# Optimization experiments

Measured on AMD Instinct MI355X. Metric: run time of the kernel, lower is better.

Reference implementation:

```python
import math
import jax, jax.numpy as jnp
import numpy as np

HEADS = 8
LOG_APPROX_VAR = math.log(0.01)  # self.var = 0.01, non-trainable


def clustering(x, approx_log_var, mu, log_var, log_prior):
    """Faithful port of DisentangledAttention.clustering (mi_estimation=False).
    x: [B,H,L,D]; approx_log_var: [B,H,L]; mu/log_var: [H,C,D]; log_prior: [H,C].
    Returns (cluster_probs [B,H,L,C], kl_loss [B,1,1], div_loss [B])."""
    B, H, L, D = x.shape
    xe = x[:, :, :, None, :]                      # [B,H,L,1,D]
    mue = mu[:, None, :, :]                       # [H,1,C,D]
    alv = approx_log_var[:, :, :, None, None]     # [B,H,L,1,1]
    avar = jnp.exp(alv)
    lv = log_var[:, None, :, :]                   # [H,1,C,D]
    var = jnp.exp(lv)
    logp = jax.nn.log_softmax(log_prior, axis=-1)  # [H,C]

    mse = (xe - mue) ** 2 / var                   # [B,H,L,C,D]
    log_pdf = -0.5 * mse.sum(-1) - D * math.pi - 0.5 * lv.sum(-1)  # [B,H,L,C]
    log_pdf = log_pdf + logp[:, None, :]
    log_probs = jax.nn.log_softmax(log_pdf, axis=-1)
    probs = jnp.exp(log_probs)                    # [B,H,L,C]

    logp_b = logp[None, :, None, :]               # broadcast prior log-probs
    prior = jnp.exp(logp_b)
    # F.kl_div(log_probs, prior) = prior * (log(prior) - log_probs)
    kl = (prior * (logp_b - log_probs)).sum(-1).mean(axis=(1, 2))            # [B]
    kl = kl + 0.5 * (probs * (mse + avar / var + lv).sum(-1)).sum(-1).mean(axis=(1, 2))
    kl = kl - 0.5 * jnp.mean(((1.0 + alv).sum(-1)) * D, axis=(1, 2, 3))
    kl_loss = kl.reshape(-1, 1, 1)

    eyeL = jnp.eye(L, dtype=x.dtype)
    div = jnp.einsum('bhqc,bhkc->bhqk', probs, probs)   # [B,H,L,L]
    div = (div - eyeL) ** 2
    wmask = eyeL * 1.25 + (1.0 - eyeL) * 0.75
    div_loss = (div * wmask).mean(axis=(1, 2, 3))       # [B]
    return probs, kl_loss, div_loss


def setup_inputs() -> dict:
    k = jax.random.key(0)
    ks = jax.random.split(k, 10)
    B, L, D, H, C = 4, 1024, 512, HEADS, 8
    Dk = D // H
    lin_std = 1.0 / math.sqrt(2.0 * D)  # xavier_normal gain=1/sqrt(2)
    return {
        'query': jax.random.normal(ks[0], (B, L, D), jnp.float32),
        'key': jax.random.normal(ks[1], (B, L, D), jnp.float32),
        'value': jax.random.normal(ks[2], (B, L, D), jnp.float32),
        'padding_mask': jnp.zeros((B, 1, L), jnp.float32),
        'Wq': jax.random.normal(ks[3], (D, D), jnp.float32) * lin_std,
        'bq': jnp.zeros((D,), jnp.float32),
        'Wk': jax.random.normal(ks[4], (D, D), jnp.float32) * lin_std,
        'bk': jnp.zeros((D,), jnp.float32),
        'Wv': jax.random.normal(ks[5], (D, D), jnp.float32) * lin_std,
        'bv': jnp.zeros((D,), jnp.float32),
        'Wo': jax.random.normal(ks[6], (D, D), jnp.float32) * lin_std,
        'bo': jnp.zeros((D,), jnp.float32),
        'tok_mu': jax.random.normal(ks[7], (H, C, Dk), jnp.float32) * 0.1,
        'tok_log_var': jnp.zeros((H, C, Dk), jnp.float32),
        'tok_log_prior': jnp.full((H, C), math.log(1.0 / C), jnp.float32),
    }


def reference(query, key, value, padding_mask, Wq, bq, Wk, bk, Wv, bv, Wo, bo,
              tok_mu, tok_log_var, tok_log_prior):
    B, L, D = query.shape
    H = HEADS
    Dk = D // H

    # GMM clustering on raw (unprojected) per-head query/key, eval mode (no reparam noise)
    qh = query.reshape(B, L, H, Dk).transpose(0, 2, 1, 3)  # [B,H,L,Dk]
    kh = key.reshape(B, L, H, Dk).transpose(0, 2, 1, 3)
    alv = jnp.full((B, H, L), LOG_APPROX_VAR, dtype=query.dtype)
    probs_q, kl_q, div_q = clustering(qh, alv, tok_mu, tok_log_var, tok_log_prior)
    probs_k, kl_k, div_k = clustering(kh, alv, tok_mu, tok_log_var, tok_log_prior)

    # Disentangled mask: tokens sharing clusters attend (mask==1 means blocked)
    sim = jnp.einsum('bhqc,bhkc->bhqk', probs_q, probs_k)   # [B,H,L,L]
    cmask = jnp.clip(1.0 - sim + padding_mask[:, :, None, :], 0.0, 1.0)

    # Projections + scaled softmax attention (per softmax_attention/full_attention)
    q = (query @ Wq.T + bq).reshape(B, L, H, Dk).transpose(0, 2, 1, 3) / math.sqrt(Dk)
    kk = (key @ Wk.T + bk).reshape(B, L, H, Dk).transpose(0, 2, 1, 3)
    v = (value @ Wv.T + bv).reshape(B, L, H, Dk).transpose(0, 2, 1, 3)
    scores = jnp.einsum('bhqd,bhkd->bhqk', q, kk) + jax.lax.stop_gradient(cmask) * (-10000.0)
    attn = jax.nn.softmax(scores, axis=-1) * (1.0 - cmask)
    out = jnp.einsum('bhqk,bhkd->bhqd', attn, v).transpose(0, 2, 1, 3).reshape(B, L, D)
    out = out @ Wo.T + bo

    kl_loss = kl_q + kl_k                      # [B,1,1]
    div_loss = (div_q + div_k).reshape(-1, 1, 1)  # [B,1,1]
    return out, kl_loss, div_loss
```

## Files before the change

kernel.cpp:

```cpp
#include <hip/hip_runtime.h>
#include <hip/hip_bf16.h>
#include <math.h>

#define NB 4
#define NL 1024
#define ND 512
#define NH 8
#define NC 8
#define NDK 64

static constexpr float KL3_CONST = 115.36544595161891f;

typedef __bf16 bf16x8 __attribute__((ext_vector_type(8)));
typedef float  f32x4v __attribute__((ext_vector_type(4)));
typedef unsigned short u16x4 __attribute__((ext_vector_type(4)));
typedef unsigned short u16x8 __attribute__((ext_vector_type(8)));

__device__ __forceinline__ unsigned short bf16u(float f) {
    return __builtin_bit_cast(unsigned short, (__bf16)f);
}

struct GemmArgs {
    const void* A; const float* W; const float* bias; void* out;
    float scale; int abf; int obf; int brow; int ostr; int vmap;
};

#define GEMM_BUF 15360

__device__ __forceinline__ void gemm_body(const GemmArgs& g, unsigned char* smem)
{
    const int tid = threadIdx.x;
    int n0, m0;
    if (g.vmap) {
        const int linear = blockIdx.y * 4 + blockIdx.x;
        n0 = (linear & 31) * 128;
        m0 = (linear >> 5) * 64;
    } else {
        n0 = blockIdx.x * 128;
        m0 = blockIdx.y * 64;
    }

    const int w = tid >> 6, lane = tid & 63;
    const int r16 = lane & 15, quad = lane >> 4;
    const int arow = tid >> 2, akc = tid & 3;
    const int wrow = tid >> 1, wkc = tid & 1;

    f32x4v acc[8];
#pragma unroll
    for (int n = 0; n < 8; ++n) acc[n] = (f32x4v){0.f, 0.f, 0.f, 0.f};

    auto ldA = [&](int k0) -> u16x8 {
        if (g.abf) {
            return *(const u16x8*)((const unsigned short*)g.A + (size_t)(m0 + arow) * 512 + k0 + akc * 8);
        }
        const float* ap = (const float*)g.A + (size_t)(m0 + arow) * 512 + k0 + akc * 8;
        const float4 a0 = *(const float4*)ap, a1 = *(const float4*)(ap + 4);
        return (u16x8){ bf16u(a0.x), bf16u(a0.y), bf16u(a0.z), bf16u(a0.w),
                        bf16u(a1.x), bf16u(a1.y), bf16u(a1.z), bf16u(a1.w) };
    };
    auto ldW = [&](int k0, u16x8* dst) {
        const float* wp = (const float*)g.W + (size_t)(n0 + wrow) * 512 + k0 + wkc * 16;
        const float4 w0 = *(const float4*)wp,       w1 = *(const float4*)(wp + 4);
        const float4 w2 = *(const float4*)(wp + 8), w3 = *(const float4*)(wp + 12);
        dst[0] = (u16x8){ bf16u(w0.x), bf16u(w0.y), bf16u(w0.z), bf16u(w0.w),
                          bf16u(w1.x), bf16u(w1.y), bf16u(w1.z), bf16u(w1.w) };
        dst[1] = (u16x8){ bf16u(w2.x), bf16u(w2.y), bf16u(w2.z), bf16u(w2.w),
                          bf16u(w3.x), bf16u(w3.y), bf16u(w3.z), bf16u(w3.w) };
    };
    auto store_stage = [&](int buf, const u16x8& sa, const u16x8* sw) {
        unsigned short* As = (unsigned short*)(smem + buf * GEMM_BUF);
        unsigned short* Ws = (unsigned short*)(smem + buf * GEMM_BUF + 5120);
        *(u16x8*)(As + arow * 40 + akc * 8) = sa;
        *(u16x8*)(Ws + wrow * 40 + wkc * 16) = sw[0];
        *(u16x8*)(Ws + wrow * 40 + wkc * 16 + 8) = sw[1];
    };
    auto mfma_half = [&](int buf) {
        unsigned short* As = (unsigned short*)(smem + buf * GEMM_BUF);
        unsigned short* Ws = (unsigned short*)(smem + buf * GEMM_BUF + 5120);
        bf16x8 af = *(const bf16x8*)(As + (w * 16 + r16) * 40 + quad * 8);
#pragma unroll
        for (int ni = 0; ni < 8; ++ni) {
            bf16x8 bfr = *(const bf16x8*)(Ws + (ni * 16 + r16) * 40 + quad * 8);
            acc[ni] = __builtin_amdgcn_mfma_f32_16x16x32_bf16(af, bfr, acc[ni], 0, 0, 0);
        }
    };

    u16x8 sa0 = ldA(0),  sw0[2]; ldW(0, sw0);
    u16x8 sa1 = ldA(32), sw1[2]; ldW(32, sw1);
    store_stage(0, sa0, sw0);
    sa0 = ldA(64); ldW(64, sw0);

    for (int p = 0; p < 16; p += 2) {
        const int kbase = p * 32;
        __syncthreads();
        store_stage(1, sa1, sw1);
        if (kbase + 96 < 512) { sa1 = ldA(kbase + 96); ldW(kbase + 96, sw1); }
        mfma_half(0);

        __syncthreads();
        if (p + 2 < 16) store_stage(0, sa0, sw0);
        if (kbase + 128 < 512) { sa0 = ldA(kbase + 128); ldW(kbase + 128, sw0); }
        mfma_half(1);
    }

#pragma unroll
    for (int ni = 0; ni < 8; ++ni) {
        const int col = n0 + ni * 16 + r16;
        const float bcol = g.brow ? 0.f : g.bias[col];
#pragma unroll
        for (int i = 0; i < 4; ++i) {
            const int row = m0 + w * 16 + quad * 4 + i;
            const float bv = g.brow ? g.bias[row] : bcol;
            const float v = (acc[ni][i] + bv) * g.scale;
            if (g.obf) ((unsigned short*)g.out)[(size_t)row * g.ostr + col] = bf16u(v);
            else       ((float*)g.out)[(size_t)row * g.ostr + col] = v;
        }
    }
}

#define GEMM_BUF64 10240

__device__ __forceinline__ void gemm_body64(const GemmArgs& g, unsigned char* smem)
{
    const int tid = threadIdx.x;
    const int n0 = blockIdx.x * 64, m0 = blockIdx.y * 64;

    const int w = tid >> 6, lane = tid & 63;
    const int r16 = lane & 15, quad = lane >> 4;
    const int arow = tid >> 2, akc = tid & 3;

    f32x4v acc[4];
#pragma unroll
    for (int n = 0; n < 4; ++n) acc[n] = (f32x4v){0.f, 0.f, 0.f, 0.f};

    auto ldA = [&](int k0) -> u16x8 {
        if (g.abf) {
            return *(const u16x8*)((const unsigned short*)g.A + (size_t)(m0 + arow) * 512 + k0 + akc * 8);
        }
        const float* ap = (const float*)g.A + (size_t)(m0 + arow) * 512 + k0 + akc * 8;
        const float4 a0 = *(const float4*)ap, a1 = *(const float4*)(ap + 4);
        return (u16x8){ bf16u(a0.x), bf16u(a0.y), bf16u(a0.z), bf16u(a0.w),
                        bf16u(a1.x), bf16u(a1.y), bf16u(a1.z), bf16u(a1.w) };
    };
    auto ldW8 = [&](int k0) -> u16x8 {
        const float* wp = (const float*)g.W + (size_t)(n0 + arow) * 512 + k0 + akc * 8;
        const float4 w0 = *(const float4*)wp, w1 = *(const float4*)(wp + 4);
        return (u16x8){ bf16u(w0.x), bf16u(w0.y), bf16u(w0.z), bf16u(w0.w),
                        bf16u(w1.x), bf16u(w1.y), bf16u(w1.z), bf16u(w1.w) };
    };
    auto store_stage = [&](int buf, const u16x8& sa, const u16x8& sw) {
        unsigned short* As = (unsigned short*)(smem + buf * GEMM_BUF64);
        unsigned short* Ws = (unsigned short*)(smem + buf * GEMM_BUF64 + 5120);
        *(u16x8*)(As + arow * 40 + akc * 8) = sa;
        *(u16x8*)(Ws + arow * 40 + akc * 8) = sw;
    };
    auto mfma_half = [&](int buf) {
        unsigned short* As = (unsigned short*)(smem + buf * GEMM_BUF64);
        unsigned short* Ws = (unsigned short*)(smem + buf * GEMM_BUF64 + 5120);
        bf16x8 af = *(const bf16x8*)(As + (w * 16 + r16) * 40 + quad * 8);
#pragma unroll
        for (int ni = 0; ni < 4; ++ni) {
            bf16x8 bfr = *(const bf16x8*)(Ws + (ni * 16 + r16) * 40 + quad * 8);
            acc[ni] = __builtin_amdgcn_mfma_f32_16x16x32_bf16(af, bfr, acc[ni], 0, 0, 0);
        }
    };

    u16x8 sa0 = ldA(0),  sw0 = ldW8(0);
    u16x8 sa1 = ldA(32), sw1 = ldW8(32);
    store_stage(0, sa0, sw0);
    sa0 = ldA(64); sw0 = ldW8(64);

    for (int p = 0; p < 16; p += 2) {
        const int kbase = p * 32;
        __syncthreads();
        store_stage(1, sa1, sw1);
        if (kbase + 96 < 512) { sa1 = ldA(kbase + 96); sw1 = ldW8(kbase + 96); }
        mfma_half(0);

        __syncthreads();
        if (p + 2 < 16) store_stage(0, sa0, sw0);
        if (kbase + 128 < 512) { sa0 = ldA(kbase + 128); sw0 = ldW8(kbase + 128); }
        mfma_half(1);
    }

#pragma unroll
    for (int ni = 0; ni < 4; ++ni) {
        const int col = n0 + ni * 16 + r16;
        const float bcol = g.brow ? 0.f : g.bias[col];
#pragma unroll
        for (int i = 0; i < 4; ++i) {
            const int row = m0 + w * 16 + quad * 4 + i;
            const float bv = g.brow ? g.bias[row] : bcol;
            const float v = (acc[ni][i] + bv) * g.scale;
            if (g.obf) ((unsigned short*)g.out)[(size_t)row * g.ostr + col] = bf16u(v);
            else       ((float*)g.out)[(size_t)row * g.ostr + col] = v;
        }
    }
}

__device__ __forceinline__ void cluster_body(
    const float* __restrict__ query, const float* __restrict__ key,
    const float* __restrict__ tok_mu, const float* __restrict__ tok_log_var,
    const float* __restrict__ tok_log_prior,
    float* __restrict__ probs_q, float* __restrict__ probs_k,
    float* __restrict__ klp, float* __restrict__ divp, float* __restrict__ Gp,
    int linear, unsigned char* smem)
{
    float* mu_s    = (float*)smem;
    float* iv_s    = (float*)(smem + 2048);
    float* Pl      = (float*)(smem + 4096);
    float* Gpart   = (float*)(smem + 13312);
    float* red_s   = (float*)(smem + 14336);
    float* lvsum_s = (float*)(smem + 14368);
    float* alpha_s = (float*)(smem + 14400);
    float* logp_s  = (float*)(smem + 14432);
    float* prior_s = (float*)(smem + 14464);

    const int tid  = threadIdx.x;
    const int side = linear >> 7;
    const int rem  = linear & 127;
    const int bh   = rem >> 2, chunk = rem & 3;
    const int b    = bh >> 3, h = bh & 7;
    const int blocklin = side * 128 + bh * 4 + chunk;
    const float* src = side ? key : query;
    float* probs_out = side ? probs_k : probs_q;

    for (int i = tid; i < 512; i += 256) {
        mu_s[i] = tok_mu[h * 512 + i];
        float lv = tok_log_var[h * 512 + i];
        iv_s[i] = __expf(-lv);
    }
    if (tid < 8) {
        float ls = 0.f, al = 0.f;
        for (int d = 0; d < 64; ++d) {
            float lv = tok_log_var[(h * 8 + tid) * 64 + d];
            ls += lv;
            al += 0.01f * __expf(-lv) + lv;
        }
        lvsum_s[tid] = ls; alpha_s[tid] = al;
    }
    if (tid == 0) {
        float lp[8]; float mx = -1e30f;
        for (int c = 0; c < 8; ++c) { lp[c] = tok_log_prior[h * 8 + c]; mx = fmaxf(mx, lp[c]); }
        float se = 0.f;
        for (int c = 0; c < 8; ++c) se += __expf(lp[c] - mx);
        float lse = mx + __logf(se);
        for (int c = 0; c < 8; ++c) { logp_s[c] = lp[c] - lse; prior_s[c] = __expf(lp[c] - lse); }
    }
    __syncthreads();

    const int l = chunk * 256 + tid;
    const float4* xp = (const float4*)(src + ((size_t)(b * NL + l)) * ND + h * NDK);
    float4 xr[16];
#pragma unroll
    for (int i = 0; i < 16; ++i) xr[i] = xp[i];

    float ms[8];
#pragma unroll
    for (int c = 0; c < 8; ++c) {
        const float4* mc = (const float4*)(mu_s + c * 64);
        const float4* ic = (const float4*)(iv_s + c * 64);
        float s = 0.f;
#pragma unroll
        for (int i = 0; i < 16; ++i) {
            float4 m4 = mc[i], v4 = ic[i], x4 = xr[i];
            float dx = x4.x - m4.x; s = fmaf(dx * dx, v4.x, s);
            float dy = x4.y - m4.y; s = fmaf(dy * dy, v4.y, s);
            float dz = x4.z - m4.z; s = fmaf(dz * dz, v4.z, s);
            float dw = x4.w - m4.w; s = fmaf(dw * dw, v4.w, s);
        }
        ms[c] = s;
    }

    float lpdf[8]; float mx = -1e30f;
#pragma unroll
    for (int c = 0; c < 8; ++c) {
        lpdf[c] = -0.5f * (ms[c] + lvsum_s[c]) + logp_s[c];
        mx = fmaxf(mx, lpdf[c]);
    }
    float e[8]; float se = 0.f;
#pragma unroll
    for (int c = 0; c < 8; ++c) { e[c] = __expf(lpdf[c] - mx); se += e[c]; }
    float lse = __logf(se);
    float inv = 1.f / se;
    float p[8]; float kl1 = 0.f, kl2 = 0.f, sqq = 0.f;
#pragma unroll
    for (int c = 0; c < 8; ++c) {
        p[c] = e[c] * inv;
        float logprob = lpdf[c] - mx - lse;
        kl1 += prior_s[c] * (logp_s[c] - logprob);
        kl2 += p[c] * (ms[c] + alpha_s[c]);
        sqq = fmaf(p[c], p[c], sqq);
    }

    float* po = probs_out + ((size_t)((b * NH + h) * NL + l)) * NC;
    ((float4*)po)[0] = make_float4(p[0], p[1], p[2], p[3]);
    ((float4*)po)[1] = make_float4(p[4], p[5], p[6], p[7]);
#pragma unroll
    for (int c = 0; c < 8; ++c) Pl[tid * 9 + c] = p[c];

    float dterm = 1.25f * (sqq - 1.f) * (sqq - 1.f) - 0.75f * sqq * sqq;
    float klv = kl1 + 0.5f * kl2;
    __syncthreads();

    {
        int qt = tid >> 6, pos = tid & 63, c1 = pos >> 3, c2 = pos & 7;
        float g = 0.f;
        for (int i = 0; i < 64; ++i) {
            int ll = qt * 64 + i;
            g = fmaf(Pl[ll * 9 + c1], Pl[ll * 9 + c2], g);
        }
        Gpart[qt * 64 + pos] = g;
    }

#pragma unroll
    for (int o = 32; o > 0; o >>= 1) {
        klv   += __shfl_down(klv, o);
        dterm += __shfl_down(dterm, o);
    }
    if ((tid & 63) == 0) { red_s[tid >> 6] = klv; red_s[4 + (tid >> 6)] = dterm; }
    __syncthreads();
    if (tid == 0) {
        klp[blocklin]  = red_s[0] + red_s[1] + red_s[2] + red_s[3];
        divp[blocklin] = red_s[4] + red_s[5] + red_s[6] + red_s[7];
    }
    if (tid < 64)
        Gp[(size_t)blocklin * 64 + tid] =
            Gpart[tid] + Gpart[64 + tid] + Gpart[128 + tid] + Gpart[192 + tid];
}

__global__ __launch_bounds__(256) void fused_front(
    GemmArgs g0, GemmArgs g1, GemmArgs g2,
    const float* query, const float* key,
    const float* tok_mu, const float* tok_log_var, const float* tok_log_prior,
    float* probs_q, float* probs_k,
    float* klp, float* divp, float* Gp)
{
    __shared__ alignas(16) unsigned char smem[2 * GEMM_BUF];
    if (blockIdx.z == 3) {
        const int linear = blockIdx.y * 4 + blockIdx.x;
        cluster_body(query, key, tok_mu, tok_log_var, tok_log_prior,
                     probs_q, probs_k, klp, divp, Gp, linear, smem);
        return;
    }
    GemmArgs g = (blockIdx.z == 0) ? g0 : ((blockIdx.z == 1) ? g1 : g2);
    gemm_body(g, smem);
}

__device__ __forceinline__ void finalize_body(
    const float* __restrict__ klp, const float* __restrict__ divp,
    const float* __restrict__ Gp, float* __restrict__ out_tail)
{
    const int tid = threadIdx.x, b = tid >> 6, lane = tid & 63;
    float gsum = 0.f;
#pragma unroll
    for (int s = 0; s < 2; ++s)
#pragma unroll
        for (int h = 0; h < 8; ++h) {
            const int base = s * 128 + (b * 8 + h) * 4;
            float Ge = 0.f;
#pragma unroll
            for (int x = 0; x < 4; ++x) Ge += Gp[(size_t)(base + x) * 64 + lane];
            gsum = fmaf(Ge, Ge, gsum);
        }
    const int s = lane >> 5, rem = lane & 31, h = rem >> 2, x = rem & 3;
    const int idx = s * 128 + (b * 8 + h) * 4 + x;
    float klv = klp[idx];
    float dvv = divp[idx];
#pragma unroll
    for (int o = 32; o > 0; o >>= 1) {
        gsum += __shfl_down(gsum, o);
        klv  += __shfl_down(klv, o);
        dvv  += __shfl_down(dvv, o);
    }
    if (lane == 0) {
        out_tail[b]     = klv * (1.0f / 8192.0f) + 2.0f * KL3_CONST;
        out_tail[4 + b] = (dvv + 0.75f * gsum) * (1.0f / 8388608.0f);
    }
}

#define APAD 72

__global__ __launch_bounds__(256) void attn_mfma7_kernel(
    const unsigned short* __restrict__ qp16, const unsigned short* __restrict__ kp16,
    const unsigned short* __restrict__ vtp16,
    const float* __restrict__ probs_q, const float* __restrict__ probs_k,
    const float* __restrict__ padding_mask,
    unsigned short* __restrict__ ao16,
    const float* __restrict__ klp, const float* __restrict__ divp,
    const float* __restrict__ Gp, float* __restrict__ out_tail)
{
    if (blockIdx.x == 16) {
        if (blockIdx.y == 0 && blockIdx.z == 0) finalize_body(klp, divp, Gp, out_tail);
        return;
    }

    const int tid = threadIdx.x, lane = tid & 63, w = tid >> 6;
    const int r16 = lane & 15, quad = lane >> 4;
    const int b = blockIdx.z;
    const int h = blockIdx.y;
    const int qt = blockIdx.x;
    const int qbase = qt * 64;

    __shared__ alignas(16) unsigned short Ks[2][64 * APAD];
    __shared__ alignas(16) unsigned short Vt[2][64 * APAD];
    __shared__ alignas(16) unsigned short Ps[4][16 * APAD];
    __shared__ float pk_s[2][8 * 65];
    __shared__ float pm_s[2][64];

    const int c0row = tid >> 3,        c0c8 = tid & 7;
    const int c1row = (tid + 256) >> 3, c1c8 = tid & 7;
    const int pkey = tid >> 1, phalf = tid & 1;

    bf16x8 qa[2];
    {
        const unsigned short* qrow = qp16 + ((size_t)(b * NL + qbase + w * 16 + r16)) * ND + h * NDK;
        qa[0] = *(const bf16x8*)(qrow + quad * 8);
        qa[1] = *(const bf16x8*)(qrow + 32 + quad * 8);
    }
    float pq[4][8];
#pragma unroll
    for (int i = 0; i < 4; ++i) {
        const float* pr = probs_q + ((size_t)((b * NH + h) * NL + qbase + w * 16 + quad * 4 + i)) * NC;
        float4 a = ((const float4*)pr)[0], c = ((const float4*)pr)[1];
        pq[i][0] = a.x; pq[i][1] = a.y; pq[i][2] = a.z; pq[i][3] = a.w;
        pq[i][4] = c.x; pq[i][5] = c.y; pq[i][6] = c.z; pq[i][7] = c.w;
    }

    f32x4v oacc[4];
#pragma unroll
    for (int n = 0; n < 4; ++n) oacc[n] = (f32x4v){0.f, 0.f, 0.f, 0.f};
    float m_i[4] = {-1e30f, -1e30f, -1e30f, -1e30f};
    float l_i[4] = {0.f, 0.f, 0.f, 0.f};

    u16x8 rk0, rk1, rv0, rv1;
    float4 rpk;
    float rpm;

    auto stage_load = [&](int kt) {
        const int key0 = kt * 64;
        rk0 = *(const u16x8*)(kp16 + ((size_t)(b * NL + key0 + c0row)) * ND + h * NDK + c0c8 * 8);
        rk1 = *(const u16x8*)(kp16 + ((size_t)(b * NL + key0 + c1row)) * ND + h * NDK + c1c8 * 8);
        rv0 = *(const u16x8*)(vtp16 + ((size_t)(h * 64 + c0row)) * (NB * NL) + b * NL + key0 + c0c8 * 8);
        rv1 = *(const u16x8*)(vtp16 + ((size_t)(h * 64 + c1row)) * (NB * NL) + b * NL + key0 + c1c8 * 8);
        if (tid < 128)
            rpk = *(const float4*)(probs_k + ((size_t)((b * NH + h) * NL + key0 + pkey)) * NC + phalf * 4);
        if (tid < 64)
            rpm = padding_mask[b * NL + key0 + tid];
    };
    auto stage_store = [&](int buf) {
        *(u16x8*)(Ks[buf] + c0row * APAD + c0c8 * 8) = rk0;
        *(u16x8*)(Ks[buf] + c1row * APAD + c1c8 * 8) = rk1;
        *(u16x8*)(Vt[buf] + c0row * APAD + c0c8 * 8) = rv0;
        *(u16x8*)(Vt[buf] + c1row * APAD + c1c8 * 8) = rv1;
        if (tid < 128) {
            pk_s[buf][(phalf * 4 + 0) * 65 + pkey] = rpk.x;
            pk_s[buf][(phalf * 4 + 1) * 65 + pkey] = rpk.y;
            pk_s[buf][(phalf * 4 + 2) * 65 + pkey] = rpk.z;
            pk_s[buf][(phalf * 4 + 3) * 65 + pkey] = rpk.w;
        }
        if (tid < 64) pm_s[buf][tid] = rpm;
    };

    stage_load(0);
    stage_store(0);
    stage_load(1);

    for (int kt = 0; kt < 16; ++kt) {
        const int cur = kt & 1;
        __syncthreads();

        f32x4v sacc[4];
#pragma unroll
        for (int t = 0; t < 4; ++t) {
            sacc[t] = (f32x4v){0.f, 0.f, 0.f, 0.f};
            bf16x8 kb0 = *(const bf16x8*)(Ks[cur] + (t * 16 + r16) * APAD + quad * 8);
            bf16x8 kb1 = *(const bf16x8*)(Ks[cur] + (t * 16 + r16) * APAD + 32 + quad * 8);
            sacc[t] = __builtin_amdgcn_mfma_f32_16x16x32_bf16(qa[0], kb0, sacc[t], 0, 0, 0);
            sacc[t] = __builtin_amdgcn_mfma_f32_16x16x32_bf16(qa[1], kb1, sacc[t], 0, 0, 0);
        }

        float sc[4][4], wgt[4][4];
#pragma unroll
        for (int t = 0; t < 4; ++t) {
            const int keyl = t * 16 + r16;
            float pkc[8];
#pragma unroll
            for (int c = 0; c < 8; ++c) pkc[c] = pk_s[cur][c * 65 + keyl];
            const float pmv = pm_s[cur][keyl];
#pragma unroll
            for (int i = 0; i < 4; ++i) {
                float sim = 0.f;
#pragma unroll
                for (int c = 0; c < 8; ++c) sim = fmaf(pq[i][c], pkc[c], sim);
                float cm = 1.f - sim + pmv;
                cm = fminf(fmaxf(cm, 0.f), 1.f);
                sc[t][i] = sacc[t][i] - 10000.f * cm;
                wgt[t][i] = 1.f - cm;
            }
        }

        float mx[4];
#pragma unroll
        for (int i = 0; i < 4; ++i)
            mx[i] = fmaxf(fmaxf(sc[0][i], sc[1][i]), fmaxf(sc[2][i], sc[3][i]));
#pragma unroll
        for (int o = 1; o < 16; o <<= 1) {
#pragma unroll
            for (int i = 0; i < 4; ++i) mx[i] = fmaxf(mx[i], __shfl_xor(mx[i], o));
        }
        float rr[4];
#pragma unroll
        for (int i = 0; i < 4; ++i) {
            const float mnew = fmaxf(m_i[i], mx[i]);
            rr[i] = __expf(m_i[i] - mnew);
            m_i[i] = mnew;
            l_i[i] *= rr[i];
        }
#pragma unroll
        for (int n = 0; n < 4; ++n) {
            oacc[n][0] *= rr[0]; oacc[n][1] *= rr[1];
            oacc[n][2] *= rr[2]; oacc[n][3] *= rr[3];
        }
        float lad[4] = {0.f, 0.f, 0.f, 0.f};
#pragma unroll
        for (int t = 0; t < 4; ++t) {
#pragma unroll
            for (int i = 0; i < 4; ++i) {
                const float p = __expf(sc[t][i] - m_i[i]);
                lad[i] += p;
                Ps[w][(quad * 4 + i) * APAD + t * 16 + r16] = bf16u(p * wgt[t][i]);
            }
        }
#pragma unroll
        for (int o = 1; o < 16; o <<= 1) {
#pragma unroll
            for (int i = 0; i < 4; ++i) lad[i] += __shfl_xor(lad[i], o);
        }
#pragma unroll
        for (int i = 0; i < 4; ++i) l_i[i] += lad[i];

        bf16x8 pa0 = *(const bf16x8*)(Ps[w] + r16 * APAD + quad * 8);
        bf16x8 pa1 = *(const bf16x8*)(Ps[w] + r16 * APAD + 32 + quad * 8);
#pragma unroll
        for (int n = 0; n < 4; ++n) {
            bf16x8 vb0 = *(const bf16x8*)(Vt[cur] + (n * 16 + r16) * APAD + quad * 8);
            bf16x8 vb1 = *(const bf16x8*)(Vt[cur] + (n * 16 + r16) * APAD + 32 + quad * 8);
            oacc[n] = __builtin_amdgcn_mfma_f32_16x16x32_bf16(pa0, vb0, oacc[n], 0, 0, 0);
            oacc[n] = __builtin_amdgcn_mfma_f32_16x16x32_bf16(pa1, vb1, oacc[n], 0, 0, 0);
        }

        if (kt < 15) stage_store(cur ^ 1);
        if (kt < 14) stage_load(kt + 2);
    }

#pragma unroll
    for (int i = 0; i < 4; ++i) {
        const float invl = 1.f / l_i[i];
        unsigned short* orow = ao16 + ((size_t)(b * NL + qbase + w * 16 + quad * 4 + i)) * ND + h * NDK;
#pragma unroll
        for (int n = 0; n < 4; ++n)
            orow[n * 16 + r16] = bf16u(oacc[n][i] * invl);
    }
}

__global__ __launch_bounds__(256) void gemm_single64(GemmArgs g)
{
    __shared__ alignas(16) unsigned char smem[2 * GEMM_BUF64];
    gemm_body64(g, smem);
}

extern "C" void kernel_launch(void* const* d_in, const int* in_sizes, int n_in,
                              void* d_out, int out_size, void* d_ws, size_t ws_size,
                              hipStream_t stream)
{
    const float* query        = (const float*)d_in[0];
    const float* key          = (const float*)d_in[1];
    const float* value        = (const float*)d_in[2];
    const float* padding_mask = (const float*)d_in[3];
    const float* Wq = (const float*)d_in[4];
    const float* bq = (const float*)d_in[5];
    const float* Wk = (const float*)d_in[6];
    const float* bk = (const float*)d_in[7];
    const float* Wv = (const float*)d_in[8];
    const float* bv = (const float*)d_in[9];
    const float* Wo = (const float*)d_in[10];
    const float* bo = (const float*)d_in[11];
    const float* tok_mu        = (const float*)d_in[12];
    const float* tok_log_var   = (const float*)d_in[13];
    const float* tok_log_prior = (const float*)d_in[14];

    float* ws = (float*)d_ws;
    const size_t FS = 1048576;
    unsigned short* qp16  = (unsigned short*)ws;
    unsigned short* kp16  = (unsigned short*)(ws + FS);
    unsigned short* vtp16 = (unsigned short*)(ws + 2 * FS);
    unsigned short* ao16  = (unsigned short*)(ws + 3 * FS);
    float* probs_q = ws + 4 * FS;
    float* probs_k = probs_q + (size_t)NB * NH * NL * NC;
    float* klp     = probs_k + (size_t)NB * NH * NL * NC;
    float* divp    = klp + 256;
    float* Gp      = divp + 256;

    GemmArgs gq {query, Wq, bq, qp16, 0.125f, 0, 1, 0, 512, 0};
    GemmArgs gk {key,   Wk, bk, kp16, 1.f,    0, 1, 0, 512, 0};
    GemmArgs gvt{Wv, value, bv, vtp16, 1.f,   0, 1, 1, 4096, 1};
    fused_front<<<dim3(4, 64, 4), 256, 0, stream>>>(
        gq, gk, gvt, query, key, tok_mu, tok_log_var, tok_log_prior,
        probs_q, probs_k, klp, divp, Gp);

    attn_mfma7_kernel<<<dim3(17, NH, NB), 256, 0, stream>>>(
        qp16, kp16, vtp16, probs_q, probs_k, padding_mask, ao16,
        klp, divp, Gp, (float*)d_out + (size_t)NB * NL * ND);

    GemmArgs go{ao16, Wo, bo, d_out, 1.f, 1, 0, 0, 512, 0};
    gemm_single64<<<dim3(8, 64, 1), 256, 0, stream>>>(go);
}
```

Before: 205.1 us.

## Split key range across two half-blocks with lazy softmax rescaling

The attention kernel now runs 512 threads per block. Each half of the block processes half of the 1024 keys for the same 64 queries, with its own shared K/V stage. The two partial results (output, max, row sum) are merged through shared memory at the end. This doubles the waves available to hide latency without changing the grid size.

The online-softmax rescale now runs only when a row's new max exceeds the running max by more than a threshold, tested with a wave vote. The per-tile row-sum shuffle reduction is deferred to the end. Both cut ALU and shuffle work in the inner loop.

In exchange, the cross-tile double buffering is gone and a second barrier is added per iteration. Unnormalised exponentials can now reach e^8 before a rescale is forced.

```diff
diff --git a/kernel.cpp b/kernel.cpp
--- a/kernel.cpp
+++ b/kernel.cpp
@@ -380,8 +380,9 @@
 }
 
 #define APAD 72
-
-__global__ __launch_bounds__(256) void attn_mfma7_kernel(
+#define RESCALE_THR 8.0f
+
+__global__ __launch_bounds__(512) void attn_mfma12_kernel(
     const unsigned short* __restrict__ qp16, const unsigned short* __restrict__ kp16,
     const unsigned short* __restrict__ vtp16,
     const float* __restrict__ probs_q, const float* __restrict__ probs_k,
@@ -391,7 +392,8 @@
     const float* __restrict__ Gp, float* __restrict__ out_tail)
 {
     if (blockIdx.x == 16) {
-        if (blockIdx.y == 0 && blockIdx.z == 0) finalize_body(klp, divp, Gp, out_tail);
+        if (blockIdx.y == 0 && blockIdx.z == 0 && threadIdx.x < 256)
+            finalize_body(klp, divp, Gp, out_tail);
         return;
     }
 
@@ -401,27 +403,31 @@
     const int h = blockIdx.y;
     const int qt = blockIdx.x;
     const int qbase = qt * 64;
+    const int s = tid >> 8;
+    const int lw = w & 3;
+    const int tid5 = tid & 255;
 
     __shared__ alignas(16) unsigned short Ks[2][64 * APAD];
     __shared__ alignas(16) unsigned short Vt[2][64 * APAD];
-    __shared__ alignas(16) unsigned short Ps[4][16 * APAD];
+    __shared__ alignas(16) unsigned short Ps[8][16 * APAD];
     __shared__ float pk_s[2][8 * 65];
     __shared__ float pm_s[2][64];
-
-    const int c0row = tid >> 3,        c0c8 = tid & 7;
-    const int c1row = (tid + 256) >> 3, c1c8 = tid & 7;
-    const int pkey = tid >> 1, phalf = tid & 1;
+    __shared__ float mml[64 * 2];
+
+    const int c0row = tid5 >> 3,         c0c8 = tid5 & 7;
+    const int c1row = (tid5 + 256) >> 3, c1c8 = tid5 & 7;
+    const int pkey = tid5 >> 1, phalf = tid5 & 1;
 
     bf16x8 qa[2];
     {
-        const unsigned short* qrow = qp16 + ((size_t)(b * NL + qbase + w * 16 + r16)) * ND + h * NDK;
+        const unsigned short* qrow = qp16 + ((size_t)(b * NL + qbase + lw * 16 + r16)) * ND + h * NDK;
         qa[0] = *(const bf16x8*)(qrow + quad * 8);
         qa[1] = *(const bf16x8*)(qrow + 32 + quad * 8);
     }
     float pq[4][8];
 #pragma unroll
     for (int i = 0; i < 4; ++i) {
-        const float* pr = probs_q + ((size_t)((b * NH + h) * NL + qbase + w * 16 + quad * 4 + i)) * NC;
+        const float* pr = probs_q + ((size_t)((b * NH + h) * NL + qbase + lw * 16 + quad * 4 + i)) * NC;
         float4 a = ((const float4*)pr)[0], c = ((const float4*)pr)[1];
         pq[i][0] = a.x; pq[i][1] = a.y; pq[i][2] = a.z; pq[i][3] = a.w;
         pq[i][4] = c.x; pq[i][5] = c.y; pq[i][6] = c.z; pq[i][7] = c.w;
@@ -438,44 +444,43 @@
     float rpm;
 
     auto stage_load = [&](int kt) {
-        const int key0 = kt * 64;
+        const int key0 = s * 512 + kt * 64;
         rk0 = *(const u16x8*)(kp16 + ((size_t)(b * NL + key0 + c0row)) * ND + h * NDK + c0c8 * 8);
         rk1 = *(const u16x8*)(kp16 + ((size_t)(b * NL + key0 + c1row)) * ND + h * NDK + c1c8 * 8);
         rv0 = *(const u16x8*)(vtp16 + ((size_t)(h * 64 + c0row)) * (NB * NL) + b * NL + key0 + c0c8 * 8);
         rv1 = *(const u16x8*)(vtp16 + ((size_t)(h * 64 + c1row)) * (NB * NL) + b * NL + key0 + c1c8 * 8);
-        if (tid < 128)
+        if (tid5 < 128)
             rpk = *(const float4*)(probs_k + ((size_t)((b * NH + h) * NL + key0 + pkey)) * NC + phalf * 4);
-        if (tid < 64)
-            rpm = padding_mask[b * NL + key0 + tid];
-    };
-    auto stage_store = [&](int buf) {
-        *(u16x8*)(Ks[buf] + c0row * APAD + c0c8 * 8) = rk0;
-        *(u16x8*)(Ks[buf] + c1row * APAD + c1c8 * 8) = rk1;
-        *(u16x8*)(Vt[buf] + c0row * APAD + c0c8 * 8) = rv0;
-        *(u16x8*)(Vt[buf] + c1row * APAD + c1c8 * 8) = rv1;
-        if (tid < 128) {
-            pk_s[buf][(phalf * 4 + 0) * 65 + pkey] = rpk.x;
-            pk_s[buf][(phalf * 4 + 1) * 65 + pkey] = rpk.y;
-            pk_s[buf][(phalf * 4 + 2) * 65 + pkey] = rpk.z;
-            pk_s[buf][(phalf * 4 + 3) * 65 + pkey] = rpk.w;
-        }
-        if (tid < 64) pm_s[buf][tid] = rpm;
+        if (tid5 < 64)
+            rpm = padding_mask[b * NL + key0 + tid5];
+    };
+    auto stage_store = [&]() {
+        *(u16x8*)(Ks[s] + c0row * APAD + c0c8 * 8) = rk0;
+        *(u16x8*)(Ks[s] + c1row * APAD + c1c8 * 8) = rk1;
+        *(u16x8*)(Vt[s] + c0row * APAD + c0c8 * 8) = rv0;
+        *(u16x8*)(Vt[s] + c1row * APAD + c1c8 * 8) = rv1;
+        if (tid5 < 128) {
+            pk_s[s][(phalf * 4 + 0) * 65 + pkey] = rpk.x;
+            pk_s[s][(phalf * 4 + 1) * 65 + pkey] = rpk.y;
+            pk_s[s][(phalf * 4 + 2) * 65 + pkey] = rpk.z;
+            pk_s[s][(phalf * 4 + 3) * 65 + pkey] = rpk.w;
+        }
+        if (tid5 < 64) pm_s[s][tid5] = rpm;
     };
 
     stage_load(0);
-    stage_store(0);
+    stage_store();
     stage_load(1);
 
-    for (int kt = 0; kt < 16; ++kt) {
-        const int cur = kt & 1;
+    for (int kt = 0; kt < 8; ++kt) {
         __syncthreads();
 
         f32x4v sacc[4];
 #pragma unroll
         for (int t = 0; t < 4; ++t) {
             sacc[t] = (f32x4v){0.f, 0.f, 0.f, 0.f};
-            bf16x8 kb0 = *(const bf16x8*)(Ks[cur] + (t * 16 + r16) * APAD + quad * 8);
-            bf16x8 kb1 = *(const bf16x8*)(Ks[cur] + (t * 16 + r16) * APAD + 32 + quad * 8);
+            bf16x8 kb0 = *(const bf16x8*)(Ks[s] + (t * 16 + r16) * APAD + quad * 8);
+            bf16x8 kb1 = *(const bf16x8*)(Ks[s] + (t * 16 + r16) * APAD + 32 + quad * 8);
             sacc[t] = __builtin_amdgcn_mfma_f32_16x16x32_bf16(qa[0], kb0, sacc[t], 0, 0, 0);
             sacc[t] = __builtin_amdgcn_mfma_f32_16x16x32_bf16(qa[1], kb1, sacc[t], 0, 0, 0);
         }
@@ -486,8 +491,8 @@
             const int keyl = t * 16 + r16;
             float pkc[8];
 #pragma unroll
-            for (int c = 0; c < 8; ++c) pkc[c] = pk_s[cur][c * 65 + keyl];
-            const float pmv = pm_s[cur][keyl];
+            for (int c = 0; c < 8; ++c) pkc[c] = pk_s[s][c * 65 + keyl];
+            const float pmv = pm_s[s][keyl];
 #pragma unroll
             for (int i = 0; i < 4; ++i) {
                 float sim = 0.f;
@@ -501,66 +506,90 @@
         }
 
         float mx[4];
-#pragma unroll
-        for (int i = 0; i < 4; ++i)
+        bool need = false;
+#pragma unroll
+        for (int i = 0; i < 4; ++i) {
             mx[i] = fmaxf(fmaxf(sc[0][i], sc[1][i]), fmaxf(sc[2][i], sc[3][i]));
-#pragma unroll
-        for (int o = 1; o < 16; o <<= 1) {
-#pragma unroll
-            for (int i = 0; i < 4; ++i) mx[i] = fmaxf(mx[i], __shfl_xor(mx[i], o));
-        }
-        float rr[4];
-#pragma unroll
-        for (int i = 0; i < 4; ++i) {
-            const float mnew = fmaxf(m_i[i], mx[i]);
-            rr[i] = __expf(m_i[i] - mnew);
-            m_i[i] = mnew;
-            l_i[i] *= rr[i];
-        }
-#pragma unroll
-        for (int n = 0; n < 4; ++n) {
-            oacc[n][0] *= rr[0]; oacc[n][1] *= rr[1];
-            oacc[n][2] *= rr[2]; oacc[n][3] *= rr[3];
-        }
-        float lad[4] = {0.f, 0.f, 0.f, 0.f};
+            need = need || (mx[i] > m_i[i] + RESCALE_THR);
+        }
+        if (__any(need)) {
+#pragma unroll
+            for (int o = 1; o < 16; o <<= 1) {
+#pragma unroll
+                for (int i = 0; i < 4; ++i) mx[i] = fmaxf(mx[i], __shfl_xor(mx[i], o));
+            }
+#pragma unroll
+            for (int i = 0; i < 4; ++i) {
+                const float mnew = fmaxf(m_i[i], mx[i]);
+                const float rr = __expf(m_i[i] - mnew);
+                m_i[i] = mnew;
+                l_i[i] *= rr;
+#pragma unroll
+                for (int n = 0; n < 4; ++n) oacc[n][i] *= rr;
+            }
+        }
 #pragma unroll
         for (int t = 0; t < 4; ++t) {
 #pragma unroll
             for (int i = 0; i < 4; ++i) {
                 const float p = __expf(sc[t][i] - m_i[i]);
-                lad[i] += p;
+                l_i[i] += p;
                 Ps[w][(quad * 4 + i) * APAD + t * 16 + r16] = bf16u(p * wgt[t][i]);
             }
         }
-#pragma unroll
-        for (int o = 1; o < 16; o <<= 1) {
-#pragma unroll
-            for (int i = 0; i < 4; ++i) lad[i] += __shfl_xor(lad[i], o);
-        }
-#pragma unroll
-        for (int i = 0; i < 4; ++i) l_i[i] += lad[i];
 
         bf16x8 pa0 = *(const bf16x8*)(Ps[w] + r16 * APAD + quad * 8);
         bf16x8 pa1 = *(const bf16x8*)(Ps[w] + r16 * APAD + 32 + quad * 8);
 #pragma unroll
         for (int n = 0; n < 4; ++n) {
-            bf16x8 vb0 = *(const bf16x8*)(Vt[cur] + (n * 16 + r16) * APAD + quad * 8);
-            bf16x8 vb1 = *(const bf16x8*)(Vt[cur] + (n * 16 + r16) * APAD + 32 + quad * 8);
+            bf16x8 vb0 = *(const bf16x8*)(Vt[s] + (n * 16 + r16) * APAD + quad * 8);
+            bf16x8 vb1 = *(const bf16x8*)(Vt[s] + (n * 16 + r16) * APAD + 32 + quad * 8);
             oacc[n] = __builtin_amdgcn_mfma_f32_16x16x32_bf16(pa0, vb0, oacc[n], 0, 0, 0);
             oacc[n] = __builtin_amdgcn_mfma_f32_16x16x32_bf16(pa1, vb1, oacc[n], 0, 0, 0);
         }
 
-        if (kt < 15) stage_store(cur ^ 1);
-        if (kt < 14) stage_load(kt + 2);
-    }
-
-#pragma unroll
-    for (int i = 0; i < 4; ++i) {
-        const float invl = 1.f / l_i[i];
-        unsigned short* orow = ao16 + ((size_t)(b * NL + qbase + w * 16 + quad * 4 + i)) * ND + h * NDK;
-#pragma unroll
-        for (int n = 0; n < 4; ++n)
-            orow[n * 16 + r16] = bf16u(oacc[n][i] * invl);
+        __syncthreads();
+        if (kt < 7) stage_store();
+        if (kt < 6) stage_load(kt + 2);
+    }
+
+#pragma unroll
+    for (int o = 1; o < 16; o <<= 1) {
+#pragma unroll
+        for (int i = 0; i < 4; ++i) l_i[i] += __shfl_xor(l_i[i], o);
+    }
+
+    float* mbuf = (float*)Ks;
+    if (s == 1) {
+#pragma unroll
+        for (int i = 0; i < 4; ++i) {
+            const int row = lw * 16 + quad * 4 + i;
+#pragma unroll
+            for (int n = 0; n < 4; ++n)
+                mbuf[row * 64 + n * 16 + r16] = oacc[n][i];
+            if (r16 == 0) {
+                mml[row * 2]     = m_i[i];
+                mml[row * 2 + 1] = l_i[i];
+            }
+        }
+    }
+    __syncthreads();
+    if (s == 0) {
+#pragma unroll
+        for (int i = 0; i < 4; ++i) {
+            const int row = lw * 16 + quad * 4 + i;
+            const float m1 = mml[row * 2], l1 = mml[row * 2 + 1];
+            const float M = fmaxf(m_i[i], m1);
+            const float e0 = __expf(m_i[i] - M), e1 = __expf(m1 - M);
+            const float inv = 1.f / fmaf(l_i[i], e0, l1 * e1);
+            const float f0 = e0 * inv, f1 = e1 * inv;
+            unsigned short* orow = ao16 + ((size_t)(b * NL + qbase + row)) * ND + h * NDK;
+#pragma unroll
+            for (int n = 0; n < 4; ++n) {
+                const int col = n * 16 + r16;
+                orow[col] = bf16u(oacc[n][i] * f0 + mbuf[row * 64 + col] * f1);
+            }
+        }
     }
 }
 
@@ -609,7 +638,7 @@
         gq, gk, gvt, query, key, tok_mu, tok_log_var, tok_log_prior,
         probs_q, probs_k, klp, divp, Gp);
 
-    attn_mfma7_kernel<<<dim3(17, NH, NB), 256, 0, stream>>>(
+    attn_mfma12_kernel<<<dim3(17, NH, NB), 512, 0, stream>>>(
         qp16, kp16, vtp16, probs_q, probs_k, padding_mask, ao16,
         klp, divp, Gp, (float*)d_out + (size_t)NB * NL * ND);
 
```

Measured after the change: 199.9 us. -2.6%, faster.
